# Kernel tuning notes

Hardware: AMD Instinct MI355X
Metric: run time of the kernel (lower is better)

The kernel has to match this reference:

```python
import jax, jax.numpy as jnp
import numpy as np

N, F, H, E, P = 2048, 128, 32, 65536, 768

def _layer_norm(v, g, b, eps=1e-5):
    mu = v.mean(-1, keepdims=True)
    var = v.var(-1, keepdims=True)
    return (v - mu) / jnp.sqrt(var + eps) * g + b

def _gcn_conv(h, src, dst, W, b, n):
    # PyG GCNConv: add self-loops, sym-normalized aggregation, then bias
    h = h @ W
    loop = jnp.arange(n)
    s = jnp.concatenate([src, loop])
    d = jnp.concatenate([dst, loop])
    deg = jax.ops.segment_sum(jnp.ones_like(s, jnp.float32), d, num_segments=n)
    dinv = jnp.where(deg > 0, deg ** -0.5, 0.0)
    msg = h[s] * (dinv[s] * dinv[d])[:, None]
    return jax.ops.segment_sum(msg, d, num_segments=n) + b

def setup_inputs():
    key = jax.random.key(0)
    ks = jax.random.split(key, 16)
    def nrm(i, shape, scale=0.05):
        return jax.random.normal(ks[i], shape, jnp.float32) * scale
    return {
        "x": jax.random.normal(ks[0], (N, F), jnp.float32),
        "ei": jax.random.randint(ks[1], (2, E), 0, N),
        "pos": jax.random.randint(ks[2], (2, P), 0, N),
        "W1": nrm(3, (F, H)), "b1": jnp.zeros((H,), jnp.float32),
        "W2": nrm(4, (H, H)), "b2": jnp.zeros((H,), jnp.float32),
        "m1_w": nrm(5, (H, H)), "m1_b": jnp.zeros((H,), jnp.float32),
        "m1_g": jnp.ones((H,), jnp.float32), "m1_beta": jnp.zeros((H,), jnp.float32),
        "m2_w": nrm(6, (H, H)), "m2_b": jnp.zeros((H,), jnp.float32),
        "m2_g": jnp.ones((H,), jnp.float32), "m2_beta": jnp.zeros((H,), jnp.float32),
        "m3_w1": nrm(7, (2 * H, H)), "m3_b1": jnp.zeros((H,), jnp.float32),
        "m3_w2": nrm(8, (H, 1)), "m3_b2": jnp.zeros((1,), jnp.float32),
    }

def reference(x, ei, pos, W1, b1, W2, b2, m1_w, m1_b, m1_g, m1_beta,
              m2_w, m2_b, m2_g, m2_beta, m3_w1, m3_b1, m3_w2, m3_b2):
    src, dst = ei[0], ei[1]
    h = _gcn_conv(x, src, dst, W1, b1, N)
    h = _gcn_conv(h, src, dst, W2, b2, N)
    xx = h[pos[0]] * h[pos[1]]          # [P,H] pair products
    xe = h[src] * h[dst]                # [E,H] edge products
    # mlp1/mlp2: Linear -> LayerNorm -> Dropout(eval: identity) -> ReLU
    x1 = jax.nn.relu(_layer_norm(xe @ m1_w + m1_b, m1_g, m1_beta))  # right factor
    x2 = jax.nn.relu(_layer_norm(xe @ m2_w + m2_b, m2_g, m2_beta))  # left factor (mlp2)
    # Scatter edge features into per-channel adjacency matrices [H,N,N]
    A1 = jnp.zeros((H, N, N), jnp.float32).at[:, src, dst].set(x2.T)
    A2 = jnp.zeros((H, N, N), jnp.float32).at[:, src, dst].set(x1.T)
    # C = bmm(A1, A2); combine() only reads C at pos pairs (zeros elsewhere),
    # so gather the needed rows/cols and contract -- identical math, no NxN output.
    rows = A1[:, pos[0], :]             # [H,P,N]
    cols = A2[:, :, pos[1]]             # [H,N,P]
    pos_val = jnp.einsum('hpn,hnp->ph', rows, cols)   # [P,H]
    z = jnp.concatenate([pos_val, xx], axis=1)        # [P,2H]
    z = jax.nn.relu(z @ m3_w1 + m3_b1)
    return (z @ m3_w2 + m3_b2).squeeze(-1)            # [P]
```

## Files before the change

### kernel.cpp

```cpp
#include <hip/hip_runtime.h>

#define N_NODES 2048
#define F_IN    128
#define HD      32
#define E_EDGES 65536
#define P_PAIRS 768

__global__ __launch_bounds__(256) void k_deg(const int* __restrict__ dst, int* __restrict__ deg) {
    int e = blockIdx.x * 256 + threadIdx.x;
    atomicAdd(&deg[dst[e]], 1);
}

__global__ __launch_bounds__(256) void k_scan(const int* __restrict__ deg, float* __restrict__ dinv,
                       int* __restrict__ offs, int* __restrict__ cursor) {
    __shared__ int ps[256];
    int tid = threadIdx.x;
    int base = tid * 8;
    int local[8]; int s = 0;
#pragma unroll
    for (int q = 0; q < 8; ++q) {
        int dg = deg[base + q];
        local[q] = s; s += dg;
        dinv[base + q] = 1.0f / sqrtf((float)(dg + 1));
    }
    ps[tid] = s; __syncthreads();
    for (int d = 1; d < 256; d <<= 1) {
        int t = (tid >= d) ? ps[tid - d] : 0;
        __syncthreads();
        ps[tid] += t;
        __syncthreads();
    }
    int excl = ps[tid] - s;
#pragma unroll
    for (int q = 0; q < 8; ++q) {
        offs[base + q]   = excl + local[q];
        cursor[base + q] = excl + local[q];
    }
    if (tid == 0) offs[N_NODES] = E_EDGES;
}

__global__ __launch_bounds__(256) void k_csr(const int* __restrict__ src, const int* __restrict__ dst,
                      const float* __restrict__ dinv,
                      int* __restrict__ cursor,
                      int* __restrict__ csr_s, float* __restrict__ csr_w) {
    int e = blockIdx.x * 256 + threadIdx.x;
    int s = src[e], d = dst[e];
    int p = atomicAdd(&cursor[d], 1);
    csr_s[p] = s;
    csr_w[p] = dinv[s] * dinv[d];
}

__global__ __launch_bounds__(256) void k_mm1(const float* __restrict__ x, const float* __restrict__ W1,
                      float* __restrict__ hW) {
    __shared__ float sW[F_IN * HD];
    int tid = threadIdx.x;
    const float4* W4 = (const float4*)W1;
    float4* s4 = (float4*)sW;
    for (int i = tid; i < F_IN * HD / 4; i += 256) s4[i] = W4[i];
    __syncthreads();
    int n = blockIdx.x * 8 + (tid >> 5), j = tid & 31;
    const float4* row = (const float4*)(x + n * F_IN);
    float acc = 0.f;
#pragma unroll
    for (int k4 = 0; k4 < F_IN / 4; ++k4) {
        float4 r = row[k4];
        acc = fmaf(r.x, sW[(k4 * 4 + 0) * HD + j], acc);
        acc = fmaf(r.y, sW[(k4 * 4 + 1) * HD + j], acc);
        acc = fmaf(r.z, sW[(k4 * 4 + 2) * HD + j], acc);
        acc = fmaf(r.w, sW[(k4 * 4 + 3) * HD + j], acc);
    }
    hW[n * HD + j] = acc;
}

__device__ __forceinline__ float csr_gather(const float* __restrict__ H,
                                            const int* __restrict__ csr_s,
                                            const float* __restrict__ csr_w,
                                            int beg, int end, int j) {
    float acc = 0.f;
    int p = beg;
    for (; p + 4 <= end; p += 4) {
        int   s0 = csr_s[p],   s1 = csr_s[p+1], s2 = csr_s[p+2], s3 = csr_s[p+3];
        float w0 = csr_w[p],   w1 = csr_w[p+1], w2 = csr_w[p+2], w3 = csr_w[p+3];
        float h0 = H[s0 * HD + j], h1 = H[s1 * HD + j];
        float h2 = H[s2 * HD + j], h3 = H[s3 * HD + j];
        acc = fmaf(h0, w0, acc);
        acc = fmaf(h1, w1, acc);
        acc = fmaf(h2, w2, acc);
        acc = fmaf(h3, w3, acc);
    }
    for (; p < end; ++p)
        acc = fmaf(H[csr_s[p] * HD + j], csr_w[p], acc);
    return acc;
}

__global__ __launch_bounds__(256) void k_gcn1mm2(const float* __restrict__ hW, const int* __restrict__ offs,
                          const int* __restrict__ csr_s, const float* __restrict__ csr_w,
                          const float* __restrict__ dinv, const float* __restrict__ b1,
                          const float* __restrict__ W2, float* __restrict__ hW2) {
    __shared__ float sW2[HD * HD];
    __shared__ float sH[8][HD];
    int tid = threadIdx.x;
    for (int i = tid; i < HD * HD; i += 256) sW2[i] = W2[i];
    __syncthreads();
    int nl = tid >> 5, j = tid & 31;
    int n = blockIdx.x * 8 + nl;
    float acc = csr_gather(hW, csr_s, csr_w, offs[n], offs[n + 1], j);
    float di = dinv[n];
    acc = fmaf(hW[n * HD + j], di * di, acc);
    sH[nl][j] = acc + b1[j];
    __syncthreads();
    float y = 0.f;
#pragma unroll
    for (int k = 0; k < HD; ++k)
        y = fmaf(sH[nl][k], sW2[k * HD + j], y);
    hW2[n * HD + j] = y;
}

__global__ __launch_bounds__(256) void k_gcn2(const float* __restrict__ hW2, const int* __restrict__ offs,
                       const int* __restrict__ csr_s, const float* __restrict__ csr_w,
                       const float* __restrict__ dinv, const float* __restrict__ b2,
                       float* __restrict__ h2) {
    int tid = threadIdx.x;
    int nl = tid >> 5, j = tid & 31;
    int n = blockIdx.x * 8 + nl;
    float acc = csr_gather(hW2, csr_s, csr_w, offs[n], offs[n + 1], j);
    float di = dinv[n];
    acc = fmaf(hW2[n * HD + j], di * di, acc);
    h2[n * HD + j] = acc + b2[j];
}

__global__ __launch_bounds__(256) void k_edge_mlp(const int* __restrict__ src, const int* __restrict__ dst,
                           const float* __restrict__ h2,
                           const float* __restrict__ m1w, const float* __restrict__ m1b,
                           const float* __restrict__ m1g, const float* __restrict__ m1be,
                           const float* __restrict__ m2w, const float* __restrict__ m2b,
                           const float* __restrict__ m2g, const float* __restrict__ m2be,
                           float* __restrict__ x1, float* __restrict__ x2,
                           int* __restrict__ eid, int* __restrict__ eidT) {
    __shared__ float s_w1[HD * HD], s_w2[HD * HD];
    int tid = threadIdx.x;
    for (int i = tid; i < HD * HD; i += 256) { s_w1[i] = m1w[i]; s_w2[i] = m2w[i]; }
    __syncthreads();
    int el = tid >> 5, j = tid & 31;
    float bb1 = m1b[j], bb2 = m2b[j];
    float g1 = m1g[j], g2 = m2g[j];
    float be1 = m1be[j], be2 = m2be[j];
#pragma unroll
    for (int it = 0; it < 8; ++it) {
        int e = blockIdx.x * 64 + it * 8 + el;
        int s = src[e], d = dst[e];
        float xe = h2[s * HD + j] * h2[d * HD + j];
        float y1 = bb1, y2 = bb2;
#pragma unroll
        for (int k = 0; k < HD; ++k) {
            float xk = __shfl(xe, k, 32);
            y1 = fmaf(xk, s_w1[k * HD + j], y1);
            y2 = fmaf(xk, s_w2[k * HD + j], y2);
        }
        float mu1 = y1, mu2 = y2;
#pragma unroll
        for (int m = 16; m > 0; m >>= 1) { mu1 += __shfl_xor(mu1, m, 32); mu2 += __shfl_xor(mu2, m, 32); }
        mu1 *= (1.f / 32.f); mu2 *= (1.f / 32.f);
        float d1 = y1 - mu1, d2 = y2 - mu2;
        float v1 = d1 * d1, v2 = d2 * d2;
#pragma unroll
        for (int m = 16; m > 0; m >>= 1) { v1 += __shfl_xor(v1, m, 32); v2 += __shfl_xor(v2, m, 32); }
        v1 *= (1.f / 32.f); v2 *= (1.f / 32.f);
        float r1 = d1 / sqrtf(v1 + 1e-5f) * g1 + be1;
        float r2 = d2 / sqrtf(v2 + 1e-5f) * g2 + be2;
        x1[e * HD + j] = fmaxf(r1, 0.f);
        x2[e * HD + j] = fmaxf(r2, 0.f);
        if (j == 0)      atomicMax(&eid [s * N_NODES + d], e);
        else if (j == 1) atomicMax(&eidT[d * N_NODES + s], e);
    }
}

__global__ __launch_bounds__(256) void k_pos(const int* __restrict__ pos, const int* __restrict__ eid,
                      const int* __restrict__ eidT,
                      const float* __restrict__ x1, const float* __restrict__ x2,
                      const float* __restrict__ h2,
                      const float* __restrict__ w1, const float* __restrict__ b1,
                      const float* __restrict__ w2, const float* __restrict__ b2,
                      float* __restrict__ out) {
    __shared__ float acc[HD];
    __shared__ float sz[2 * HD];
    int p = blockIdx.x;
    int i = pos[p], j = pos[P_PAIRS + p];
    int tid = threadIdx.x;
    if (tid < HD) acc[tid] = 0.f;
    __syncthreads();
    const int4* rowA = (const int4*)(eid  + (size_t)i * N_NODES);
    const int4* rowB = (const int4*)(eidT + (size_t)j * N_NODES);
    for (int q = tid; q < N_NODES / 4; q += 256) {
        int4 ea = rowA[q];
        int4 eb = rowB[q];
        int e1[4] = { ea.x, ea.y, ea.z, ea.w };
        int e2[4] = { eb.x, eb.y, eb.z, eb.w };
#pragma unroll
        for (int u = 0; u < 4; ++u) {
            if ((e1[u] | e2[u]) >= 0) {
                const float4* a4 = (const float4*)(x2 + (size_t)e1[u] * HD);
                const float4* b4 = (const float4*)(x1 + (size_t)e2[u] * HD);
#pragma unroll
                for (int q4 = 0; q4 < HD / 4; ++q4) {
                    float4 av = a4[q4], bv = b4[q4];
                    atomicAdd(&acc[q4 * 4 + 0], av.x * bv.x);
                    atomicAdd(&acc[q4 * 4 + 1], av.y * bv.y);
                    atomicAdd(&acc[q4 * 4 + 2], av.z * bv.z);
                    atomicAdd(&acc[q4 * 4 + 3], av.w * bv.w);
                }
            }
        }
    }
    __syncthreads();
    if (tid < HD) {
        sz[tid] = acc[tid];
        sz[HD + tid] = h2[i * HD + tid] * h2[j * HD + tid];
    }
    __syncthreads();
    if (tid < HD) {
        float t = b1[tid];
#pragma unroll
        for (int k = 0; k < 2 * HD; ++k) t = fmaf(sz[k], w1[k * HD + tid], t);
        t = fmaxf(t, 0.f);
        float r = t * w2[tid];
#pragma unroll
        for (int m = 16; m > 0; m >>= 1) r += __shfl_xor(r, m, 32);
        if (tid == 0) out[p] = r + b2[0];
    }
}

extern "C" void kernel_launch(void* const* d_in, const int* in_sizes, int n_in,
                              void* d_out, int out_size, void* d_ws, size_t ws_size,
                              hipStream_t stream) {
    const float* x     = (const float*)d_in[0];
    const int*   ei    = (const int*)d_in[1];
    const int*   pos   = (const int*)d_in[2];
    const float* W1    = (const float*)d_in[3];
    const float* b1    = (const float*)d_in[4];
    const float* W2    = (const float*)d_in[5];
    const float* b2    = (const float*)d_in[6];
    const float* m1w   = (const float*)d_in[7];
    const float* m1b   = (const float*)d_in[8];
    const float* m1g   = (const float*)d_in[9];
    const float* m1be  = (const float*)d_in[10];
    const float* m2w   = (const float*)d_in[11];
    const float* m2b   = (const float*)d_in[12];
    const float* m2g   = (const float*)d_in[13];
    const float* m2be  = (const float*)d_in[14];
    const float* m3w1  = (const float*)d_in[15];
    const float* m3b1  = (const float*)d_in[16];
    const float* m3w2  = (const float*)d_in[17];
    const float* m3b2  = (const float*)d_in[18];

    const int* src = ei;
    const int* dst = ei + E_EDGES;

    char* w = (char*)d_ws;
    size_t off = 0;
    auto alloc = [&](size_t bytes) { void* p = w + off; off += (bytes + 255) & ~size_t(255); return p; };
    int*   deg    = (int*)  alloc(N_NODES * 4);
    float* dinv   = (float*)alloc(N_NODES * 4);
    int*   offs   = (int*)  alloc((N_NODES + 1) * 4);
    int*   cursor = (int*)  alloc(N_NODES * 4);
    int*   csr_s  = (int*)  alloc((size_t)E_EDGES * 4);
    float* csr_w  = (float*)alloc((size_t)E_EDGES * 4);
    float* hW     = (float*)alloc((size_t)N_NODES * HD * 4);
    float* hW2    = (float*)alloc((size_t)N_NODES * HD * 4);
    float* h2     = (float*)alloc((size_t)N_NODES * HD * 4);
    float* x1     = (float*)alloc((size_t)E_EDGES * HD * 4);
    float* x2     = (float*)alloc((size_t)E_EDGES * HD * 4);
    int*   eid    = (int*)  alloc((size_t)N_NODES * N_NODES * 4);
    int*   eidT   = (int*)  alloc((size_t)N_NODES * N_NODES * 4);

    hipMemsetAsync(deg, 0, N_NODES * 4, stream);

    k_deg<<<E_EDGES / 256, 256, 0, stream>>>(dst, deg);
    k_scan<<<1, 256, 0, stream>>>(deg, dinv, offs, cursor);
    k_csr<<<E_EDGES / 256, 256, 0, stream>>>(src, dst, dinv, cursor, csr_s, csr_w);

    k_mm1<<<N_NODES / 8, 256, 0, stream>>>(x, W1, hW);
    k_gcn1mm2<<<N_NODES / 8, 256, 0, stream>>>(hW, offs, csr_s, csr_w, dinv, b1, W2, hW2);
    k_gcn2<<<N_NODES / 8, 256, 0, stream>>>(hW2, offs, csr_s, csr_w, dinv, b2, h2);

    k_edge_mlp<<<E_EDGES / 64, 256, 0, stream>>>(src, dst, h2,
        m1w, m1b, m1g, m1be, m2w, m2b, m2g, m2be, x1, x2, eid, eidT);

    k_pos<<<P_PAIRS, 256, 0, stream>>>(pos, eid, eidT, x1, x2, h2,
                                       m3w1, m3b1, m3w2, m3b2, (float*)d_out);
}
```

Baseline: 172.9 us.

## Compute edge MLP lazily only for matched edge pairs inside pair kernel

Removes the edge-wide MLP kernel and its two E×H intermediate buffers. Instead, the pair kernel first collects matching (e1,e2) edge pairs into a shared-memory queue, then runs both Linear+LayerNorm+ReLU MLPs only for those edges. The eid/eidT scatter moves into the CSR build kernel, and the degree count is fused with the first matmul into one launch. This trades a large streaming write and a full-edge compute pass for redundant per-pair recomputation and a larger shared-memory footprint in the pair kernel.

```diff
diff --git a/kernel.cpp b/kernel.cpp
--- a/kernel.cpp
+++ b/kernel.cpp
@@ -6,9 +6,35 @@
 #define E_EDGES 65536
 #define P_PAIRS 768
 
-__global__ __launch_bounds__(256) void k_deg(const int* __restrict__ dst, int* __restrict__ deg) {
-    int e = blockIdx.x * 256 + threadIdx.x;
-    atomicAdd(&deg[dst[e]], 1);
+__global__ __launch_bounds__(256) void k_deg_mm1(const int* __restrict__ dst,
+                                                 int* __restrict__ deg,
+                                                 const float* __restrict__ x,
+                                                 const float* __restrict__ W1,
+                                                 float* __restrict__ hW) {
+    __shared__ float sW[F_IN * HD];
+    int tid = threadIdx.x;
+    int bid = blockIdx.x;
+    if (bid < 256) {
+        int e = bid * 256 + tid;
+        atomicAdd(&deg[dst[e]], 1);
+        return;
+    }
+    const float4* W4 = (const float4*)W1;
+    float4* s4 = (float4*)sW;
+    for (int i = tid; i < F_IN * HD / 4; i += 256) s4[i] = W4[i];
+    __syncthreads();
+    int n = (bid - 256) * 8 + (tid >> 5), j = tid & 31;
+    const float4* row = (const float4*)(x + n * F_IN);
+    float acc = 0.f;
+#pragma unroll
+    for (int k4 = 0; k4 < F_IN / 4; ++k4) {
+        float4 r = row[k4];
+        acc = fmaf(r.x, sW[(k4 * 4 + 0) * HD + j], acc);
+        acc = fmaf(r.y, sW[(k4 * 4 + 1) * HD + j], acc);
+        acc = fmaf(r.z, sW[(k4 * 4 + 2) * HD + j], acc);
+        acc = fmaf(r.w, sW[(k4 * 4 + 3) * HD + j], acc);
+    }
+    hW[n * HD + j] = acc;
 }
 
 __global__ __launch_bounds__(256) void k_scan(const int* __restrict__ deg, float* __restrict__ dinv,
@@ -42,34 +68,15 @@
 __global__ __launch_bounds__(256) void k_csr(const int* __restrict__ src, const int* __restrict__ dst,
                       const float* __restrict__ dinv,
                       int* __restrict__ cursor,
-                      int* __restrict__ csr_s, float* __restrict__ csr_w) {
+                      int* __restrict__ csr_s, float* __restrict__ csr_w,
+                      int* __restrict__ eid, int* __restrict__ eidT) {
     int e = blockIdx.x * 256 + threadIdx.x;
     int s = src[e], d = dst[e];
     int p = atomicAdd(&cursor[d], 1);
     csr_s[p] = s;
     csr_w[p] = dinv[s] * dinv[d];
-}
-
-__global__ __launch_bounds__(256) void k_mm1(const float* __restrict__ x, const float* __restrict__ W1,
-                      float* __restrict__ hW) {
-    __shared__ float sW[F_IN * HD];
-    int tid = threadIdx.x;
-    const float4* W4 = (const float4*)W1;
-    float4* s4 = (float4*)sW;
-    for (int i = tid; i < F_IN * HD / 4; i += 256) s4[i] = W4[i];
-    __syncthreads();
-    int n = blockIdx.x * 8 + (tid >> 5), j = tid & 31;
-    const float4* row = (const float4*)(x + n * F_IN);
-    float acc = 0.f;
-#pragma unroll
-    for (int k4 = 0; k4 < F_IN / 4; ++k4) {
-        float4 r = row[k4];
-        acc = fmaf(r.x, sW[(k4 * 4 + 0) * HD + j], acc);
-        acc = fmaf(r.y, sW[(k4 * 4 + 1) * HD + j], acc);
-        acc = fmaf(r.z, sW[(k4 * 4 + 2) * HD + j], acc);
-        acc = fmaf(r.w, sW[(k4 * 4 + 3) * HD + j], acc);
-    }
-    hW[n * HD + j] = acc;
+    atomicMax(&eid [(size_t)s * N_NODES + d], e);
+    atomicMax(&eidT[(size_t)d * N_NODES + s], e);
 }
 
 __device__ __forceinline__ float csr_gather(const float* __restrict__ H,
@@ -129,93 +136,86 @@
     h2[n * HD + j] = acc + b2[j];
 }
 
-__global__ __launch_bounds__(256) void k_edge_mlp(const int* __restrict__ src, const int* __restrict__ dst,
-                           const float* __restrict__ h2,
-                           const float* __restrict__ m1w, const float* __restrict__ m1b,
-                           const float* __restrict__ m1g, const float* __restrict__ m1be,
-                           const float* __restrict__ m2w, const float* __restrict__ m2b,
-                           const float* __restrict__ m2g, const float* __restrict__ m2be,
-                           float* __restrict__ x1, float* __restrict__ x2,
-                           int* __restrict__ eid, int* __restrict__ eidT) {
-    __shared__ float s_w1[HD * HD], s_w2[HD * HD];
-    int tid = threadIdx.x;
-    for (int i = tid; i < HD * HD; i += 256) { s_w1[i] = m1w[i]; s_w2[i] = m2w[i]; }
-    __syncthreads();
-    int el = tid >> 5, j = tid & 31;
-    float bb1 = m1b[j], bb2 = m2b[j];
-    float g1 = m1g[j], g2 = m2g[j];
-    float be1 = m1be[j], be2 = m2be[j];
-#pragma unroll
-    for (int it = 0; it < 8; ++it) {
-        int e = blockIdx.x * 64 + it * 8 + el;
-        int s = src[e], d = dst[e];
-        float xe = h2[s * HD + j] * h2[d * HD + j];
-        float y1 = bb1, y2 = bb2;
-#pragma unroll
-        for (int k = 0; k < HD; ++k) {
-            float xk = __shfl(xe, k, 32);
-            y1 = fmaf(xk, s_w1[k * HD + j], y1);
-            y2 = fmaf(xk, s_w2[k * HD + j], y2);
-        }
-        float mu1 = y1, mu2 = y2;
-#pragma unroll
-        for (int m = 16; m > 0; m >>= 1) { mu1 += __shfl_xor(mu1, m, 32); mu2 += __shfl_xor(mu2, m, 32); }
-        mu1 *= (1.f / 32.f); mu2 *= (1.f / 32.f);
-        float d1 = y1 - mu1, d2 = y2 - mu2;
-        float v1 = d1 * d1, v2 = d2 * d2;
-#pragma unroll
-        for (int m = 16; m > 0; m >>= 1) { v1 += __shfl_xor(v1, m, 32); v2 += __shfl_xor(v2, m, 32); }
-        v1 *= (1.f / 32.f); v2 *= (1.f / 32.f);
-        float r1 = d1 / sqrtf(v1 + 1e-5f) * g1 + be1;
-        float r2 = d2 / sqrtf(v2 + 1e-5f) * g2 + be2;
-        x1[e * HD + j] = fmaxf(r1, 0.f);
-        x2[e * HD + j] = fmaxf(r2, 0.f);
-        if (j == 0)      atomicMax(&eid [s * N_NODES + d], e);
-        else if (j == 1) atomicMax(&eidT[d * N_NODES + s], e);
-    }
-}
-
-__global__ __launch_bounds__(256) void k_pos(const int* __restrict__ pos, const int* __restrict__ eid,
-                      const int* __restrict__ eidT,
-                      const float* __restrict__ x1, const float* __restrict__ x2,
+__global__ __launch_bounds__(256) void k_pos(const int* __restrict__ pos,
+                      const int* __restrict__ eid, const int* __restrict__ eidT,
+                      const int* __restrict__ src, const int* __restrict__ dst,
                       const float* __restrict__ h2,
+                      const float* __restrict__ m1w, const float* __restrict__ m1b,
+                      const float* __restrict__ m1g, const float* __restrict__ m1be,
+                      const float* __restrict__ m2w, const float* __restrict__ m2b,
+                      const float* __restrict__ m2g, const float* __restrict__ m2be,
                       const float* __restrict__ w1, const float* __restrict__ b1,
                       const float* __restrict__ w2, const float* __restrict__ b2,
                       float* __restrict__ out) {
+    __shared__ float s_w1[HD * HD], s_w2[HD * HD];
+    __shared__ int2  q[N_NODES];
+    __shared__ int   qn;
     __shared__ float acc[HD];
     __shared__ float sz[2 * HD];
     int p = blockIdx.x;
-    int i = pos[p], j = pos[P_PAIRS + p];
-    int tid = threadIdx.x;
+    int i = pos[p], jn = pos[P_PAIRS + p];
+    int tid = threadIdx.x;
+    for (int t = tid; t < HD * HD; t += 256) { s_w1[t] = m1w[t]; s_w2[t] = m2w[t]; }
+    if (tid == 0) qn = 0;
     if (tid < HD) acc[tid] = 0.f;
     __syncthreads();
-    const int4* rowA = (const int4*)(eid  + (size_t)i * N_NODES);
-    const int4* rowB = (const int4*)(eidT + (size_t)j * N_NODES);
-    for (int q = tid; q < N_NODES / 4; q += 256) {
-        int4 ea = rowA[q];
-        int4 eb = rowB[q];
+
+    const int4* rowA = (const int4*)(eid  + (size_t)i  * N_NODES);
+    const int4* rowB = (const int4*)(eidT + (size_t)jn * N_NODES);
+    for (int t = tid; t < N_NODES / 4; t += 256) {
+        int4 ea = rowA[t];
+        int4 eb = rowB[t];
         int e1[4] = { ea.x, ea.y, ea.z, ea.w };
         int e2[4] = { eb.x, eb.y, eb.z, eb.w };
 #pragma unroll
         for (int u = 0; u < 4; ++u) {
             if ((e1[u] | e2[u]) >= 0) {
-                const float4* a4 = (const float4*)(x2 + (size_t)e1[u] * HD);
-                const float4* b4 = (const float4*)(x1 + (size_t)e2[u] * HD);
-#pragma unroll
-                for (int q4 = 0; q4 < HD / 4; ++q4) {
-                    float4 av = a4[q4], bv = b4[q4];
-                    atomicAdd(&acc[q4 * 4 + 0], av.x * bv.x);
-                    atomicAdd(&acc[q4 * 4 + 1], av.y * bv.y);
-                    atomicAdd(&acc[q4 * 4 + 2], av.z * bv.z);
-                    atomicAdd(&acc[q4 * 4 + 3], av.w * bv.w);
-                }
+                int slot = atomicAdd(&qn, 1);
+                q[slot] = make_int2(e1[u], e2[u]);
             }
         }
     }
     __syncthreads();
+
+    int nmatch = qn;
+    int wave = tid >> 6;
+    int j = tid & 31;
+    float bb1 = m1b[j], bb2 = m2b[j];
+    float g1v = m1g[j], g2v = m2g[j];
+    float be1 = m1be[j], be2 = m2be[j];
+    for (int m = wave; m < nmatch; m += 4) {
+        int2 me = q[m];
+        int e1 = me.x, e2 = me.y;
+        int s1 = src[e1], d1 = dst[e1];
+        int s2 = src[e2], d2 = dst[e2];
+        float xeA = h2[s1 * HD + j] * h2[d1 * HD + j];
+        float xeB = h2[s2 * HD + j] * h2[d2 * HD + j];
+        float yA = bb2, yB = bb1;
+#pragma unroll
+        for (int k = 0; k < HD; ++k) {
+            float ka = __shfl(xeA, k, 32);
+            float kb = __shfl(xeB, k, 32);
+            yA = fmaf(ka, s_w2[k * HD + j], yA);
+            yB = fmaf(kb, s_w1[k * HD + j], yB);
+        }
+        float muA = yA, muB = yB;
+#pragma unroll
+        for (int mm = 16; mm > 0; mm >>= 1) { muA += __shfl_xor(muA, mm, 32); muB += __shfl_xor(muB, mm, 32); }
+        muA *= (1.f / 32.f); muB *= (1.f / 32.f);
+        float dA = yA - muA, dB = yB - muB;
+        float vA = dA * dA, vB = dB * dB;
+#pragma unroll
+        for (int mm = 16; mm > 0; mm >>= 1) { vA += __shfl_xor(vA, mm, 32); vB += __shfl_xor(vB, mm, 32); }
+        vA *= (1.f / 32.f); vB *= (1.f / 32.f);
+        float x2v = fmaxf(dA / sqrtf(vA + 1e-5f) * g2v + be2, 0.f);
+        float x1v = fmaxf(dB / sqrtf(vB + 1e-5f) * g1v + be1, 0.f);
+        if ((tid & 63) < 32) atomicAdd(&acc[j], x2v * x1v);
+    }
+    __syncthreads();
+
     if (tid < HD) {
         sz[tid] = acc[tid];
-        sz[HD + tid] = h2[i * HD + tid] * h2[j * HD + tid];
+        sz[HD + tid] = h2[i * HD + tid] * h2[jn * HD + tid];
     }
     __syncthreads();
     if (tid < HD) {
@@ -225,7 +225,7 @@
         t = fmaxf(t, 0.f);
         float r = t * w2[tid];
 #pragma unroll
-        for (int m = 16; m > 0; m >>= 1) r += __shfl_xor(r, m, 32);
+        for (int mm = 16; mm > 0; mm >>= 1) r += __shfl_xor(r, mm, 32);
         if (tid == 0) out[p] = r + b2[0];
     }
 }
@@ -268,24 +268,19 @@
     float* hW     = (float*)alloc((size_t)N_NODES * HD * 4);
     float* hW2    = (float*)alloc((size_t)N_NODES * HD * 4);
     float* h2     = (float*)alloc((size_t)N_NODES * HD * 4);
-    float* x1     = (float*)alloc((size_t)E_EDGES * HD * 4);
-    float* x2     = (float*)alloc((size_t)E_EDGES * HD * 4);
     int*   eid    = (int*)  alloc((size_t)N_NODES * N_NODES * 4);
     int*   eidT   = (int*)  alloc((size_t)N_NODES * N_NODES * 4);
 
     hipMemsetAsync(deg, 0, N_NODES * 4, stream);
 
-    k_deg<<<E_EDGES / 256, 256, 0, stream>>>(dst, deg);
+    k_deg_mm1<<<512, 256, 0, stream>>>(dst, deg, x, W1, hW);
     k_scan<<<1, 256, 0, stream>>>(deg, dinv, offs, cursor);
-    k_csr<<<E_EDGES / 256, 256, 0, stream>>>(src, dst, dinv, cursor, csr_s, csr_w);
-
-    k_mm1<<<N_NODES / 8, 256, 0, stream>>>(x, W1, hW);
+    k_csr<<<E_EDGES / 256, 256, 0, stream>>>(src, dst, dinv, cursor, csr_s, csr_w, eid, eidT);
+
     k_gcn1mm2<<<N_NODES / 8, 256, 0, stream>>>(hW, offs, csr_s, csr_w, dinv, b1, W2, hW2);
     k_gcn2<<<N_NODES / 8, 256, 0, stream>>>(hW2, offs, csr_s, csr_w, dinv, b2, h2);
 
-    k_edge_mlp<<<E_EDGES / 64, 256, 0, stream>>>(src, dst, h2,
-        m1w, m1b, m1g, m1be, m2w, m2b, m2g, m2be, x1, x2, eid, eidT);
-
-    k_pos<<<P_PAIRS, 256, 0, stream>>>(pos, eid, eidT, x1, x2, h2,
+    k_pos<<<P_PAIRS, 256, 0, stream>>>(pos, eid, eidT, src, dst, h2,
+                                       m1w, m1b, m1g, m1be, m2w, m2b, m2g, m2be,
                                        m3w1, m3b1, m3w2, m3b2, (float*)d_out);
 }
```

After: 142.3 us. 17.7% less time.
